# Kernel tuning notes

Measured on AMD Instinct MI355X. Metric: run time of the kernel, lower is better.

Reference implementation:

```python
import jax, jax.numpy as jnp
import numpy as np

T, H, N, D = 4096, 16, 16, 64


def setup_inputs() -> dict:
    key = jax.random.key(0)
    ks = jax.random.split(key, 8)
    x = jax.random.normal(ks[0], (T, H, D), dtype=jnp.float32)
    dt = jax.random.uniform(ks[1], (T, H), dtype=jnp.float32) * 0.1  # small positive timesteps
    B = jax.random.normal(ks[2], (T, H, N), dtype=jnp.float32)
    C = jax.random.normal(ks[3], (T, H, N), dtype=jnp.float32)
    mask = jax.random.randint(ks[4], (T,), 0, 2).astype(jnp.float32)  # reset flags in {0,1}
    initial_carry = jax.random.normal(ks[5], (H, N, D), dtype=jnp.float32)
    log_decay = jax.random.normal(ks[6], (H,), dtype=jnp.float32) * 0.1
    skip_weight = jnp.ones((H, D), dtype=jnp.float32)
    return {"x": x, "dt": dt, "B": B, "C": C, "mask": mask,
            "initial_carry": initial_carry, "log_decay": log_decay,
            "skip_weight": skip_weight}


def _binary_operator(q_i, q_j):
    # elementwise; broadcasting replaces the original per-time vmap
    a_i, b_i, c_i = q_i
    a_j, b_j, c_j = q_j
    a_out = a_j * a_i * (1.0 - c_j) + a_j * c_j
    b_out = (a_j * b_i + b_j) * (1.0 - c_j) + b_j * c_j
    c_out = c_i * (1.0 - c_j) + c_j
    return (a_out, b_out, c_out)


def reference(x, dt, B, C, mask, initial_carry, log_decay, skip_weight):
    num_heads = dt.shape[1]
    decay_rate = -jnp.exp(log_decay)                        # [H]
    decay_factor = jnp.exp(dt * decay_rate[None, :])        # [T,H]
    decay_factor = decay_factor[:, :, None, None]           # [T,H,1,1]
    decay_factor = jnp.concatenate(
        [jnp.ones((1, num_heads, 1, 1), dtype=decay_factor.dtype), decay_factor], axis=0)
    driving_input = jnp.einsum('th,thn,thd->thnd', dt, B, x)  # [T,H,N,D]
    driving_input = jnp.concatenate([initial_carry[None, ...], driving_input], axis=0)
    m = jnp.concatenate([jnp.zeros((1,), dtype=mask.dtype), mask])
    m = m[:, None, None, None]                              # [T+1,1,1,1]
    _, hidden_states, _ = jax.lax.associative_scan(
        _binary_operator, (decay_factor, driving_input, m))
    next_carry = hidden_states[-1]                          # [H,N,D]
    valid_states = hidden_states[1:]                        # [T,H,N,D]
    output = jnp.einsum('thn,thnd->thd', C, valid_states)   # [T,H,D]
    output = output + skip_weight[None, :, :] * x
    return (next_carry, output)
```

## Files before the change

### kernel.cpp

```cpp
#include <hip/hip_runtime.h>

#define T_LEN 4096
#define H 16
#define N 16
#define D 64
#define NC 256
#define CL (T_LEN / NC)

static __device__ __forceinline__ unsigned short f2bf(float f) {
    union { float f; unsigned u; } v; v.f = f;
    unsigned r = (v.u + 0x7fffu + ((v.u >> 16) & 1u)) >> 16;
    return (unsigned short)r;
}
static __device__ __forceinline__ float bf2f(unsigned short s) {
    union { unsigned u; float f; } v; v.u = ((unsigned)s) << 16;
    return v.f;
}

__global__ __launch_bounds__(64)
void phase1(const float* __restrict__ x, const float* __restrict__ dt,
            const float* __restrict__ B, const float* __restrict__ mask,
            const float* __restrict__ log_decay,
            unsigned short* __restrict__ Lb, float* __restrict__ Pbuf) {
    const int c = blockIdx.x, h = blockIdx.y;
    const int d = threadIdx.x;
    const float rate = -__expf(log_decay[h]);
    const int t0 = c * CL;

    __shared__ float Bs[CL * N];
    {
        const float4* Bg = (const float4*)B;
        float4* Bsv = (float4*)Bs;
        const int j = d;
        const int row = j >> 2, off = j & 3;
        const float dtv = dt[(t0 + row) * H + h];
        float4 bv = Bg[((t0 + row) * H + h) * (N / 4) + off];
        bv.x *= dtv; bv.y *= dtv; bv.z *= dtv; bv.w *= dtv;
        Bsv[j] = bv;
    }
    __syncthreads();

    float s[N];
#pragma unroll
    for (int n = 0; n < N; ++n) s[n] = 0.f;
    float P = 1.f;

#pragma unroll
    for (int ss = 0; ss < CL; ++ss) {
        const int t = t0 + ss;
        const float dtv = dt[t * H + h];
        const float mv  = mask[t];
        const float a   = (1.f - mv) * __expf(dtv * rate);
        const float xv  = x[(t * H + h) * D + d];
        P *= a;
        const float4* Br4 = (const float4*)(Bs + ss * N);
#pragma unroll
        for (int q = 0; q < 4; ++q) {
            const float4 bv = Br4[q];
            s[4*q+0] = a * s[4*q+0] + bv.x * xv;
            s[4*q+1] = a * s[4*q+1] + bv.y * xv;
            s[4*q+2] = a * s[4*q+2] + bv.z * xv;
            s[4*q+3] = a * s[4*q+3] + bv.w * xv;
        }
    }

    unsigned short* Lp = Lb + ((c * H + h) * N) * D + d;
#pragma unroll
    for (int n = 0; n < N; ++n) Lp[n * D] = f2bf(s[n]);
    if (d == 0) Pbuf[h * NC + c] = P;
}

__global__ __launch_bounds__(256)
void phase2(const float* __restrict__ initial_carry,
            unsigned short* __restrict__ LE, const float* __restrict__ Pbuf,
            float* __restrict__ next_carry) {
    const int idx = blockIdx.x * 256 + threadIdx.x;
    const int h = blockIdx.x >> 2;
    float carry = initial_carry[idx];

#pragma unroll
    for (int r = 0; r < NC / 64; ++r) {
        float l[64];
#pragma unroll
        for (int k = 0; k < 64; ++k)
            l[k] = bf2f(LE[(r * 64 + k) * (H * N * D) + idx]);
#pragma unroll
        for (int k = 0; k < 64; ++k) {
            const float p = Pbuf[h * NC + r * 64 + k];
            LE[(r * 64 + k) * (H * N * D) + idx] = f2bf(carry);
            carry = p * carry + l[k];
        }
    }
    next_carry[idx] = carry;
}

__global__ __launch_bounds__(64)
void phase3(const float* __restrict__ x, const float* __restrict__ dt,
            const float* __restrict__ B, const float* __restrict__ C,
            const float* __restrict__ mask, const float* __restrict__ log_decay,
            const float* __restrict__ skip_weight,
            const unsigned short* __restrict__ Eb, float* __restrict__ out) {
    const int c = blockIdx.x, h = blockIdx.y;
    const int d = threadIdx.x;
    const float rate = -__expf(log_decay[h]);
    const int t0 = c * CL;

    __shared__ float Bs[CL * N], Cs[CL * N];
    {
        const float4* Bg = (const float4*)B;
        const float4* Cg = (const float4*)C;
        float4* Bsv = (float4*)Bs;
        float4* Csv = (float4*)Cs;
        const int j = d;
        const int row = j >> 2, off = j & 3;
        const float dtv = dt[(t0 + row) * H + h];
        float4 bv = Bg[((t0 + row) * H + h) * (N / 4) + off];
        bv.x *= dtv; bv.y *= dtv; bv.z *= dtv; bv.w *= dtv;
        Bsv[j] = bv;
        Csv[j] = Cg[((t0 + row) * H + h) * (N / 4) + off];
    }
    __syncthreads();

    float s[N];
    const unsigned short* Ep = Eb + ((c * H + h) * N) * D + d;
#pragma unroll
    for (int n = 0; n < N; ++n) s[n] = bf2f(Ep[n * D]);

    const float sw = skip_weight[h * D + d];
#pragma unroll
    for (int ss = 0; ss < CL; ++ss) {
        const int t = t0 + ss;
        const float dtv = dt[t * H + h];
        const float mv  = mask[t];
        const float a   = (1.f - mv) * __expf(dtv * rate);
        const float xv  = x[(t * H + h) * D + d];
        float acc = sw * xv;
        const float4* Br4 = (const float4*)(Bs + ss * N);
        const float4* Cr4 = (const float4*)(Cs + ss * N);
#pragma unroll
        for (int q = 0; q < 4; ++q) {
            const float4 bv = Br4[q];
            const float4 cv = Cr4[q];
            s[4*q+0] = a * s[4*q+0] + bv.x * xv;  acc += cv.x * s[4*q+0];
            s[4*q+1] = a * s[4*q+1] + bv.y * xv;  acc += cv.y * s[4*q+1];
            s[4*q+2] = a * s[4*q+2] + bv.z * xv;  acc += cv.z * s[4*q+2];
            s[4*q+3] = a * s[4*q+3] + bv.w * xv;  acc += cv.w * s[4*q+3];
        }
        __builtin_nontemporal_store(acc, &out[(t * H + h) * D + d]);
    }
}

extern "C" void kernel_launch(void* const* d_in, const int* in_sizes, int n_in,
                              void* d_out, int out_size, void* d_ws, size_t ws_size,
                              hipStream_t stream) {
    const float* x    = (const float*)d_in[0];
    const float* dt   = (const float*)d_in[1];
    const float* B    = (const float*)d_in[2];
    const float* C    = (const float*)d_in[3];
    const float* mask = (const float*)d_in[4];
    const float* ic   = (const float*)d_in[5];
    const float* ld   = (const float*)d_in[6];
    const float* sw   = (const float*)d_in[7];
    float* out = (float*)d_out;

    float* Pbuf = (float*)d_ws;
    unsigned short* Lb = (unsigned short*)((char*)d_ws + 16384);

    dim3 grid(NC, H), block(64);
    phase1<<<grid, block, 0, stream>>>(x, dt, B, mask, ld, Lb, Pbuf);
    phase2<<<dim3(H * N * D / 256), dim3(256), 0, stream>>>(ic, Lb, Pbuf, out);
    phase3<<<grid, block, 0, stream>>>(x, dt, B, C, mask, ld, sw, Lb, out + H * N * D);
}
```

Before: 38.29 us.

## Compute local chunk outputs in phase one and apply carry correction afterwards

The first kernel now also computes each chunk's output from a zero initial state, including the skip term, and writes it to a workspace buffer. The final kernel no longer rescans B and x. It adds a correction equal to the cumulative decay times C dotted with the incoming carry. The combine kernel processes 128 chunks per unrolled batch inside a non-unrolled outer loop. This moves the recurrence work off the last kernel, at the cost of an extra fp32 write and read of the full output-sized buffer.

```diff
diff --git a/kernel.cpp b/kernel.cpp
--- a/kernel.cpp
+++ b/kernel.cpp
@@ -6,6 +6,7 @@
 #define D 64
 #define NC 256
 #define CL (T_LEN / NC)
+#define HND (H * N * D)
 
 static __device__ __forceinline__ unsigned short f2bf(float f) {
     union { float f; unsigned u; } v; v.f = f;
@@ -18,31 +19,35 @@
 }
 
 __global__ __launch_bounds__(64)
-void phase1(const float* __restrict__ x, const float* __restrict__ dt,
-            const float* __restrict__ B, const float* __restrict__ mask,
-            const float* __restrict__ log_decay,
-            unsigned short* __restrict__ Lb, float* __restrict__ Pbuf) {
+void k1_local(const float* __restrict__ x, const float* __restrict__ dt,
+              const float* __restrict__ B, const float* __restrict__ C,
+              const float* __restrict__ mask, const float* __restrict__ log_decay,
+              const float* __restrict__ skip_weight,
+              unsigned short* __restrict__ Lb, float* __restrict__ Pbuf,
+              float* __restrict__ OL) {
     const int c = blockIdx.x, h = blockIdx.y;
     const int d = threadIdx.x;
     const float rate = -__expf(log_decay[h]);
     const int t0 = c * CL;
 
-    __shared__ float Bs[CL * N];
+    __shared__ float Bs[CL * N], Cs[CL * N];
     {
         const float4* Bg = (const float4*)B;
-        float4* Bsv = (float4*)Bs;
+        const float4* Cg = (const float4*)C;
         const int j = d;
         const int row = j >> 2, off = j & 3;
         const float dtv = dt[(t0 + row) * H + h];
         float4 bv = Bg[((t0 + row) * H + h) * (N / 4) + off];
         bv.x *= dtv; bv.y *= dtv; bv.z *= dtv; bv.w *= dtv;
-        Bsv[j] = bv;
+        ((float4*)Bs)[j] = bv;
+        ((float4*)Cs)[j] = Cg[((t0 + row) * H + h) * (N / 4) + off];
     }
     __syncthreads();
 
     float s[N];
 #pragma unroll
     for (int n = 0; n < N; ++n) s[n] = 0.f;
+    const float swv = skip_weight[h * D + d];
     float P = 1.f;
 
 #pragma unroll
@@ -53,88 +58,7 @@
         const float a   = (1.f - mv) * __expf(dtv * rate);
         const float xv  = x[(t * H + h) * D + d];
         P *= a;
-        const float4* Br4 = (const float4*)(Bs + ss * N);
-#pragma unroll
-        for (int q = 0; q < 4; ++q) {
-            const float4 bv = Br4[q];
-            s[4*q+0] = a * s[4*q+0] + bv.x * xv;
-            s[4*q+1] = a * s[4*q+1] + bv.y * xv;
-            s[4*q+2] = a * s[4*q+2] + bv.z * xv;
-            s[4*q+3] = a * s[4*q+3] + bv.w * xv;
-        }
-    }
-
-    unsigned short* Lp = Lb + ((c * H + h) * N) * D + d;
-#pragma unroll
-    for (int n = 0; n < N; ++n) Lp[n * D] = f2bf(s[n]);
-    if (d == 0) Pbuf[h * NC + c] = P;
-}
-
-__global__ __launch_bounds__(256)
-void phase2(const float* __restrict__ initial_carry,
-            unsigned short* __restrict__ LE, const float* __restrict__ Pbuf,
-            float* __restrict__ next_carry) {
-    const int idx = blockIdx.x * 256 + threadIdx.x;
-    const int h = blockIdx.x >> 2;
-    float carry = initial_carry[idx];
-
-#pragma unroll
-    for (int r = 0; r < NC / 64; ++r) {
-        float l[64];
-#pragma unroll
-        for (int k = 0; k < 64; ++k)
-            l[k] = bf2f(LE[(r * 64 + k) * (H * N * D) + idx]);
-#pragma unroll
-        for (int k = 0; k < 64; ++k) {
-            const float p = Pbuf[h * NC + r * 64 + k];
-            LE[(r * 64 + k) * (H * N * D) + idx] = f2bf(carry);
-            carry = p * carry + l[k];
-        }
-    }
-    next_carry[idx] = carry;
-}
-
-__global__ __launch_bounds__(64)
-void phase3(const float* __restrict__ x, const float* __restrict__ dt,
-            const float* __restrict__ B, const float* __restrict__ C,
-            const float* __restrict__ mask, const float* __restrict__ log_decay,
-            const float* __restrict__ skip_weight,
-            const unsigned short* __restrict__ Eb, float* __restrict__ out) {
-    const int c = blockIdx.x, h = blockIdx.y;
-    const int d = threadIdx.x;
-    const float rate = -__expf(log_decay[h]);
-    const int t0 = c * CL;
-
-    __shared__ float Bs[CL * N], Cs[CL * N];
-    {
-        const float4* Bg = (const float4*)B;
-        const float4* Cg = (const float4*)C;
-        float4* Bsv = (float4*)Bs;
-        float4* Csv = (float4*)Cs;
-        const int j = d;
-        const int row = j >> 2, off = j & 3;
-        const float dtv = dt[(t0 + row) * H + h];
-        float4 bv = Bg[((t0 + row) * H + h) * (N / 4) + off];
-        bv.x *= dtv; bv.y *= dtv; bv.z *= dtv; bv.w *= dtv;
-        Bsv[j] = bv;
-        Csv[j] = Cg[((t0 + row) * H + h) * (N / 4) + off];
-    }
-    __syncthreads();
-
-    float s[N];
-    const unsigned short* Ep = Eb + ((c * H + h) * N) * D + d;
-#pragma unroll
-    for (int n = 0; n < N; ++n) s[n] = bf2f(Ep[n * D]);
-
-    const float sw = skip_weight[h * D + d];
-#pragma unroll
-    for (int ss = 0; ss < CL; ++ss) {
-        const int t = t0 + ss;
-        const float dtv = dt[t * H + h];
-        const float mv  = mask[t];
-        const float a   = (1.f - mv) * __expf(dtv * rate);
-        const float xv  = x[(t * H + h) * D + d];
-        float acc = sw * xv;
+        float acc = swv * xv;
         const float4* Br4 = (const float4*)(Bs + ss * N);
         const float4* Cr4 = (const float4*)(Cs + ss * N);
 #pragma unroll
@@ -146,7 +70,82 @@
             s[4*q+2] = a * s[4*q+2] + bv.z * xv;  acc += cv.z * s[4*q+2];
             s[4*q+3] = a * s[4*q+3] + bv.w * xv;  acc += cv.w * s[4*q+3];
         }
-        __builtin_nontemporal_store(acc, &out[(t * H + h) * D + d]);
+        OL[(t * H + h) * D + d] = acc;
+    }
+
+    unsigned short* Lp = Lb + ((size_t)(c * H + h) * N) * D + d;
+#pragma unroll
+    for (int n = 0; n < N; ++n) Lp[n * D] = f2bf(s[n]);
+    if (d == 0) Pbuf[h * NC + c] = P;
+}
+
+__global__ __launch_bounds__(256)
+void k2_combine(const float* __restrict__ initial_carry,
+                unsigned short* __restrict__ LE, const float* __restrict__ Pbuf,
+                float* __restrict__ next_carry) {
+    const int idx = blockIdx.x * 256 + threadIdx.x;
+    const int h = blockIdx.x >> 2;
+    float carry = initial_carry[idx];
+
+#pragma unroll 1
+    for (int r = 0; r < NC / 128; ++r) {
+        float l[128];
+#pragma unroll
+        for (int k = 0; k < 128; ++k)
+            l[k] = bf2f(LE[(size_t)(r * 128 + k) * HND + idx]);
+#pragma unroll
+        for (int k = 0; k < 128; ++k) {
+            const float p = Pbuf[h * NC + r * 128 + k];
+            LE[(size_t)(r * 128 + k) * HND + idx] = f2bf(carry);
+            carry = p * carry + l[k];
+        }
+    }
+    next_carry[idx] = carry;
+}
+
+__global__ __launch_bounds__(64)
+void k3_correct(const float* __restrict__ dt, const float* __restrict__ C,
+                const float* __restrict__ mask, const float* __restrict__ log_decay,
+                const unsigned short* __restrict__ Eb,
+                const float* __restrict__ OL, float* __restrict__ out) {
+    const int c = blockIdx.x, h = blockIdx.y;
+    const int d = threadIdx.x;
+    const float rate = -__expf(log_decay[h]);
+    const int t0 = c * CL;
+
+    __shared__ float Cs[CL * N];
+    {
+        const float4* Cg = (const float4*)C;
+        const int j = d;
+        const int row = j >> 2, off = j & 3;
+        ((float4*)Cs)[j] = Cg[((t0 + row) * H + h) * (N / 4) + off];
+    }
+    __syncthreads();
+
+    float E[N];
+    {
+        const unsigned short* Ep = Eb + ((size_t)(c * H + h) * N) * D + d;
+#pragma unroll
+        for (int n = 0; n < N; ++n) E[n] = bf2f(Ep[n * D]);
+    }
+
+    float pa = 1.f;
+#pragma unroll
+    for (int ss = 0; ss < CL; ++ss) {
+        const int t = t0 + ss;
+        const float dtv = dt[t * H + h];
+        const float mv  = mask[t];
+        pa *= (1.f - mv) * __expf(dtv * rate);
+        const float4* Cr4 = (const float4*)(Cs + ss * N);
+        float corr = 0.f;
+#pragma unroll
+        for (int q = 0; q < 4; ++q) {
+            const float4 cv = Cr4[q];
+            corr += cv.x * E[4*q+0] + cv.y * E[4*q+1]
+                  + cv.z * E[4*q+2] + cv.w * E[4*q+3];
+        }
+        const float ol = OL[(t * H + h) * D + d];
+        __builtin_nontemporal_store(ol + pa * corr, &out[(t * H + h) * D + d]);
     }
 }
 
@@ -165,9 +164,10 @@
 
     float* Pbuf = (float*)d_ws;
     unsigned short* Lb = (unsigned short*)((char*)d_ws + 16384);
+    float* OL = (float*)((char*)d_ws + 16384 + (size_t)NC * HND * 2);
 
     dim3 grid(NC, H), block(64);
-    phase1<<<grid, block, 0, stream>>>(x, dt, B, mask, ld, Lb, Pbuf);
-    phase2<<<dim3(H * N * D / 256), dim3(256), 0, stream>>>(ic, Lb, Pbuf, out);
-    phase3<<<grid, block, 0, stream>>>(x, dt, B, C, mask, ld, sw, Lb, out + H * N * D);
+    k1_local<<<grid, block, 0, stream>>>(x, dt, B, C, mask, ld, sw, Lb, Pbuf, OL);
+    k2_combine<<<dim3(HND / 256), dim3(256), 0, stream>>>(ic, Lb, Pbuf, out);
+    k3_correct<<<grid, block, 0, stream>>>(dt, C, mask, ld, Lb, OL, out + HND);
 }
```

New measurement: 38.71 us. No clear change (+1.1%).
